# Kernel optimization log

Hardware: AMD Instinct MI355X
Metric: run time of the kernel (lower is better)

The kernel has to match this reference:

```python
import jax, jax.numpy as jnp
import numpy as np

COEF_MEMORY = 0.2

def setup_inputs() -> dict:
    key = jax.random.key(0)
    k1, k2, k3, k4 = jax.random.split(key, 4)
    B, T, HW, C, Cv, M = 2, 8, 4096, 64, 3, 1024
    k = jax.random.normal(k1, (B, T, HW, C), dtype=jnp.float32)
    v = jax.random.normal(k2, (B, T, HW, Cv), dtype=jnp.float32)
    m_k = jax.random.normal(k3, (B, T - 1, M, C), dtype=jnp.float32)
    m_v = jax.random.normal(k4, (B, T - 1, M, Cv), dtype=jnp.float32)
    return {"k": k, "v": v, "m_k": m_k, "m_v": m_v}

def reference(k, v, m_k, m_v):
    # k: [B,T,HW,C] frame keys; v: [B,T,HW,Cv] frame values (quarter-res images)
    # m_k: [B,T-1,M,C] memory keys at step i; m_v: [B,T-1,M,Cv] memory values
    c = COEF_MEMORY
    k_i = k[:, :-1]  # ref keys  [B,T-1,HW,C]
    k_j = k[:, 1:]   # tar keys  [B,T-1,HW,C]
    v_i = v[:, :-1]  # ref vals  [B,T-1,HW,Cv]
    # frame-to-frame affinity: softmax over ref positions (last axis)
    sim_k = jax.nn.softmax(jnp.einsum('btqc,btkc->btqk', k_j, k_i), axis=-1)
    # memory-to-frame affinity: softmax over memory slots
    sim_m = jax.nn.softmax(jnp.einsum('btqc,btmc->btqm', k_j, m_k), axis=-1)
    rec_k = jnp.einsum('btqk,btkd->btqd', sim_k, v_i)   # [B,T-1,HW,Cv]
    rec_m = jnp.einsum('btqm,btmd->btqd', sim_m, m_v)   # [B,T-1,HW,Cv]
    return (1.0 - c) * rec_k + c * rec_m
```

## Files before the change

### kernel.cpp

```cpp
#include <hip/hip_runtime.h>

typedef __attribute__((ext_vector_type(2))) __fp16 h2;
typedef __attribute__((ext_vector_type(4))) __fp16 h4;
typedef __attribute__((ext_vector_type(8))) __fp16 h8;
typedef __attribute__((ext_vector_type(4))) float f32x4;

#define LOG2E 1.44269504088896340736f

#define WS_K    0ull
#define WS_MK   7340032ull
#define WS_VT   9175040ull
#define WS_MVT  9633792ull
#define WS_NEED 9748480ull

__device__ __forceinline__ h2 pkrtz(float a, float b) {
    return __builtin_bit_cast(h2, __builtin_amdgcn_cvt_pkrtz(a, b));
}

__device__ __forceinline__ void gll16(const void* g, void* l) {
    __builtin_amdgcn_global_load_lds(
        (const __attribute__((address_space(1))) unsigned int*)g,
        (__attribute__((address_space(3))) unsigned int*)l, 16, 0, 0);
}

__global__ __launch_bounds__(256) void kast_pre_kernel(
    const float* __restrict__ K, const float* __restrict__ V,
    const float* __restrict__ MK, const float* __restrict__ MV,
    char* __restrict__ ws)
{
    const int id = blockIdx.x * 256 + threadIdx.x;
    if (id < 573440) {
        const bool ismk = id >= 458752;
        const int lid = ismk ? id - 458752 : id;
        const int c = lid & 7;
        const int r = (lid >> 3) & 63;
        int kt, s;
        if (ismk) { kt = (lid >> 9) & 15; s = lid >> 13; }
        else      { kt = (lid >> 9) & 63; s = lid >> 15; }
        const int b = s / 7, t = s - b * 7;
        const float* src = ismk
            ? MK + (((size_t)(b * 7 + t) * 1024 + kt * 64 + r) * 64 + c * 8)
            : K  + (((size_t)(b * 8 + t) * 4096 + kt * 64 + r) * 64 + c * 8);
        const f32x4 xa = *(const f32x4*)src;
        const f32x4 xb = *(const f32x4*)(src + 4);
        const h2 q0 = pkrtz(xa[0], xa[1]), q1 = pkrtz(xa[2], xa[3]);
        const h2 q2 = pkrtz(xb[0], xb[1]), q3 = pkrtz(xb[2], xb[3]);
        const h8 out = {q0[0], q0[1], q1[0], q1[1], q2[0], q2[1], q3[0], q3[1]};
        __fp16* dst = (__fp16*)(ws + (ismk ? WS_MK : WS_K))
                    + (size_t)(ismk ? (s * 16 + kt) : (s * 64 + kt)) * 4096
                    + r * 64 + ((c ^ (r & 7)) * 8);
        *(h8*)dst = out;
    } else {
        const int vid = id - 573440;
        const bool ismv = vid >= 57344;
        const int lid = ismv ? vid - 57344 : vid;
        const int c = lid & 15;
        const int d = (lid >> 4) & 3;
        int kt, s;
        if (ismv) { kt = (lid >> 6) & 15; s = lid >> 10; }
        else      { kt = (lid >> 6) & 63; s = lid >> 12; }
        const int b = s / 7, t = s - b * 7;
        const float* src = ismv
            ? MV + (((size_t)(b * 7 + t) * 1024 + kt * 64 + c * 4) * 3)
            : V  + (((size_t)(b * 8 + t) * 4096 + kt * 64 + c * 4) * 3);
        float f0, f1, f2, f3;
        if (d == 3) { f0 = f1 = f2 = f3 = 1.0f; }
        else { f0 = src[d]; f1 = src[3 + d]; f2 = src[6 + d]; f3 = src[9 + d]; }
        const h2 pa = pkrtz(f0, f1), pb = pkrtz(f2, f3);
        const h4 out4 = {pa[0], pa[1], pb[0], pb[1]};
        __fp16* dst = (__fp16*)(ws + (ismv ? WS_MVT : WS_VT))
                    + (size_t)(ismv ? (s * 16 + kt) : (s * 64 + kt)) * 256
                    + d * 64 + (4 * ((c >> 2) ^ d) + (c & 3)) * 4;
        *(h4*)dst = out4;
    }
}

__global__ __launch_bounds__(512) void kast_attn_kernel(
    const float* __restrict__ K,
    const char* __restrict__ ws,
    float* __restrict__ OUT)
{
    __shared__ alignas(16) __fp16 sK2[2][2][64][64];
    __shared__ alignas(16) __fp16 sVT2[2][2][4][64];
    __shared__ float mrg[8][32][5];

    const int id = blockIdx.x;
    const int sw = (id & 7) * 112 + (id >> 3);
    const int bt = sw >> 6;
    const int qblk = sw & 63;
    const int b = bt / 7, t = bt - b * 7;

    const int tid = threadIdx.x;
    const int lane = tid & 63;
    const int w = tid >> 6;
    const int h = w >> 2;
    const int wl = w & 3;
    const int qsub = wl >> 1;
    const int ntp = wl & 1;
    const int col = lane & 15;
    const int g = lane >> 4;
    const int cs = col & 7;
    const int d3 = col & 3;

    h8 aq[2][2];
#pragma unroll
    for (int mt = 0; mt < 2; ++mt) {
        const float* qp = K + (((size_t)b * 8 + (t + 1)) * 4096
                         + (size_t)(qblk * 64 + qsub * 32 + mt * 16 + col)) * 64;
#pragma unroll
        for (int ch = 0; ch < 2; ++ch) {
            const int cc = ch * 32 + g * 8;
            const f32x4 xa = *(const f32x4*)&qp[cc];
            const f32x4 xb = *(const f32x4*)&qp[cc + 4];
            const h2 p0 = pkrtz(xa[0] * LOG2E, xa[1] * LOG2E);
            const h2 p1 = pkrtz(xa[2] * LOG2E, xa[3] * LOG2E);
            const h2 p2 = pkrtz(xb[0] * LOG2E, xb[1] * LOG2E);
            const h2 p3 = pkrtz(xb[2] * LOG2E, xb[3] * LOG2E);
            aq[mt][ch] = (h8){p0[0], p0[1], p1[0], p1[1], p2[0], p2[1], p3[0], p3[1]};
        }
    }

    auto stage = [&](const char* kb, const char* vb, int tkt, int buf) {
        const char* ksrc = kb + (size_t)tkt * 8192 + wl * 2048 + lane * 16;
        char* kdst = ((char*)&sK2[h][buf][0][0]) + wl * 2048 + lane * 16;
        gll16(ksrc, kdst);
        gll16(ksrc + 1024, kdst + 1024);
        if (wl == 0 && lane < 32)
            ((f32x4*)&sVT2[h][buf][0][0])[lane] =
                ((const f32x4*)(vb + (size_t)tkt * 512))[lane];
    };

    float oa0 = 0.f, oa1 = 0.f, oa2 = 0.f;

#pragma unroll
    for (int phase = 0; phase < 2; ++phase) {
        const char* kbase; const char* vbase; int ntile; float wgt;
        if (phase == 0) {
            ntile = 32; wgt = 0.8f;
            kbase = ws + WS_K  + ((size_t)bt * 64 + h * 32) * 8192;
            vbase = ws + WS_VT + ((size_t)bt * 64 + h * 32) * 512;
        } else {
            ntile = 8; wgt = 0.2f;
            kbase = ws + WS_MK  + ((size_t)bt * 16 + h * 8) * 8192;
            vbase = ws + WS_MVT + ((size_t)bt * 16 + h * 8) * 512;
        }

        stage(kbase, vbase, 0, 0);
        __syncthreads();

        float mrun[2] = {-1e30f, -1e30f};
        f32x4 O[2] = {(f32x4){0.f,0.f,0.f,0.f}, (f32x4){0.f,0.f,0.f,0.f}};

        for (int kt = 0; kt < ntile; ++kt) {
            const int cur = kt & 1;

            if (kt + 1 < ntile) stage(kbase, vbase, kt + 1, cur ^ 1);

            f32x4 acc[2][2];
#pragma unroll
            for (int mt = 0; mt < 2; ++mt)
#pragma unroll
                for (int nt = 0; nt < 2; ++nt) acc[mt][nt] = (f32x4){0.f,0.f,0.f,0.f};
            __builtin_amdgcn_s_setprio(1);
#pragma unroll
            for (int ch = 0; ch < 2; ++ch) {
                h8 bh[2];
#pragma unroll
                for (int nt = 0; nt < 2; ++nt) {
                    const int nt2 = ntp * 2 + nt;
                    bh[nt] = *(const h8*)&sK2[h][cur][nt2 * 16 + col][((ch * 4 + g) ^ cs) * 8];
                }
#pragma unroll
                for (int mt = 0; mt < 2; ++mt)
#pragma unroll
                    for (int nt = 0; nt < 2; ++nt)
                        acc[mt][nt] = __builtin_amdgcn_mfma_f32_16x16x32_f16(bh[nt], aq[mt][ch], acc[mt][nt], 0, 0, 0);
            }
            __builtin_amdgcn_s_setprio(0);

            const char* vtb = (const char*)&sVT2[h][cur][0][0] + d3 * 128;
#pragma unroll
            for (int mt = 0; mt < 2; ++mt) {
                float tm = acc[mt][0][0];
#pragma unroll
                for (int nt = 0; nt < 2; ++nt)
#pragma unroll
                    for (int j = 0; j < 4; ++j) tm = fmaxf(tm, acc[mt][nt][j]);
                tm = fmaxf(tm, __shfl_xor(tm, 16));
                tm = fmaxf(tm, __shfl_xor(tm, 32));
                if (!__all(tm <= mrun[mt])) {
                    const float mnew = fmaxf(mrun[mt], tm);
                    const float sc = __builtin_amdgcn_exp2f(mrun[mt] - mnew);
                    O[mt] *= sc;
                    mrun[mt] = mnew;
                }
#pragma unroll
                for (int nt = 0; nt < 2; ++nt) {
                    const int nt2 = ntp * 2 + nt;
                    const float p0 = __builtin_amdgcn_exp2f(acc[mt][nt][0] - mrun[mt]);
                    const float p1 = __builtin_amdgcn_exp2f(acc[mt][nt][1] - mrun[mt]);
                    const float p2 = __builtin_amdgcn_exp2f(acc[mt][nt][2] - mrun[mt]);
                    const float p3 = __builtin_amdgcn_exp2f(acc[mt][nt][3] - mrun[mt]);
                    const h2 pa = pkrtz(p0, p1), pb = pkrtz(p2, p3);
                    const h4 pf = (h4){pa[0], pa[1], pb[0], pb[1]};
                    const h4 vf = *(const h4*)(vtb + (4 * (nt2 ^ d3) + g) * 8);
                    O[mt] = __builtin_amdgcn_mfma_f32_16x16x16f16(vf, pf, O[mt], 0, 0, 0);
                }
            }

            __syncthreads();
        }

        if (g == 0) {
#pragma unroll
            for (int mt = 0; mt < 2; ++mt) {
                float* m5 = &mrg[w][mt * 16 + col][0];
                m5[0] = mrun[mt];
                m5[1] = O[mt][0]; m5[2] = O[mt][1]; m5[3] = O[mt][2]; m5[4] = O[mt][3];
            }
        }
        __syncthreads();
        if (tid < 64) {
            const int qh = tid >> 5, ql = tid & 31;
            float m = -1e30f;
#pragma unroll
            for (int c = 0; c < 4; ++c) {
                const int w4 = (c >> 1) * 4 + qh * 2 + (c & 1);
                m = fmaxf(m, mrg[w4][ql][0]);
            }
            float l = 0.f, r0 = 0.f, r1 = 0.f, r2 = 0.f;
#pragma unroll
            for (int c = 0; c < 4; ++c) {
                const int w4 = (c >> 1) * 4 + qh * 2 + (c & 1);
                const float* m5 = &mrg[w4][ql][0];
                const float e = __builtin_amdgcn_exp2f(m5[0] - m);
                r0 += m5[1] * e; r1 += m5[2] * e; r2 += m5[3] * e;
                l  += m5[4] * e;
            }
            const float inv = wgt / l;
            oa0 += r0 * inv; oa1 += r1 * inv; oa2 += r2 * inv;
        }
    }

    if (tid < 64) {
        const int q = qblk * 64 + tid;
        float* op = OUT + (((size_t)b * 7 + t) * 4096 + (size_t)q) * 3;
        op[0] = oa0; op[1] = oa1; op[2] = oa2;
    }
}

__global__ __launch_bounds__(256) void kast_attn_fb(
    const float* __restrict__ K, const float* __restrict__ V,
    const float* __restrict__ MK, const float* __restrict__ MV,
    float* __restrict__ OUT)
{
    __shared__ alignas(16) __fp16 sK[2][64][64];
    __shared__ alignas(16) __fp16 sVT[2][4][68];

    const int id = blockIdx.x;
    const int sw = (id & 7) * 112 + (id >> 3);
    const int bt = sw >> 6;
    const int qblk = sw & 63;
    const int b = bt / 7, t = bt % 7;

    const int tid = threadIdx.x;
    const int lane = tid & 63;
    const int w = tid >> 6;
    const int col = lane & 15;
    const int g = lane >> 4;

    const int r = tid >> 2;
    const int c0 = (tid & 3) * 16;
    const int rs = (r & 7) << 3;
    const unsigned vr = (unsigned)tid / 3u;
    const unsigned vd = (unsigned)tid - vr * 3u;

    if (tid < 128) sVT[tid >> 6][3][tid & 63] = (__fp16)1.0f;

    const float* Qbase = K + (((size_t)b * 8 + (t + 1)) * 4096) * 64;
    h8 aq[2];
    {
        const int qrow = qblk * 64 + w * 16 + col;
        const float* qp = Qbase + (size_t)qrow * 64;
#pragma unroll
        for (int ch = 0; ch < 2; ++ch) {
            const int cc = ch * 32 + g * 8;
            const f32x4 xa = *(const f32x4*)&qp[cc];
            const f32x4 xb = *(const f32x4*)&qp[cc + 4];
            const h2 p0 = pkrtz(xa[0] * LOG2E, xa[1] * LOG2E);
            const h2 p1 = pkrtz(xa[2] * LOG2E, xa[3] * LOG2E);
            const h2 p2 = pkrtz(xb[0] * LOG2E, xb[1] * LOG2E);
            const h2 p3 = pkrtz(xb[2] * LOG2E, xb[3] * LOG2E);
            aq[ch] = (h8){p0[0], p0[1], p1[0], p1[1], p2[0], p2[1], p3[0], p3[1]};
        }
    }

    float outc0 = 0.f, outc1 = 0.f, outc2 = 0.f;

    for (int phase = 0; phase < 2; ++phase) {
        const float* kp; const float* vp; int ntile; float wgt;
        if (phase == 0) {
            kp = K + (((size_t)b * 8 + t) * 4096) * 64;
            vp = V + (((size_t)b * 8 + t) * 4096) * 3;
            ntile = 64; wgt = 0.8f;
        } else {
            kp = MK + (((size_t)b * 7 + t) * 1024) * 64;
            vp = MV + (((size_t)b * 7 + t) * 1024) * 3;
            ntile = 16; wgt = 0.2f;
        }
        {
            const float* src = kp + ((size_t)r) * 64 + c0;
            const f32x4* s4 = (const f32x4*)src;
            const f32x4 ra = s4[0], rb = s4[1], rc = s4[2], rd = s4[3];
            const h2 q0 = pkrtz(ra[0], ra[1]), q1 = pkrtz(ra[2], ra[3]);
            const h2 q2 = pkrtz(rb[0], rb[1]), q3 = pkrtz(rb[2], rb[3]);
            const h2 q4 = pkrtz(rc[0], rc[1]), q5 = pkrtz(rc[2], rc[3]);
            const h2 q6 = pkrtz(rd[0], rd[1]), q7 = pkrtz(rd[2], rd[3]);
            *(h8*)&sK[0][r][c0 ^ rs] = (h8){q0[0], q0[1], q1[0], q1[1], q2[0], q2[1], q3[0], q3[1]};
            *(h8*)&sK[0][r][(c0 + 8) ^ rs] = (h8){q4[0], q4[1], q5[0], q5[1], q6[0], q6[1], q7[0], q7[1]};
            if (tid < 192) sVT[0][vd][vr] = (__fp16)vp[tid];
        }
        __syncthreads();

        float mrun = -1e30f;
        f32x4 O = (f32x4){0.f, 0.f, 0.f, 0.f};

        for (int kt = 0; kt < ntile; ++kt) {
            const int cur = kt & 1;
            const bool have = (kt + 1) < ntile;
            f32x4 ra, rb, rc, rd; float rv = 0.f;
            if (have) {
                const float* src = kp + ((size_t)(kt + 1) * 64 + r) * 64 + c0;
                const f32x4* s4 = (const f32x4*)src;
                ra = s4[0]; rb = s4[1]; rc = s4[2]; rd = s4[3];
                if (tid < 192) rv = vp[(size_t)(kt + 1) * 192 + tid];
            }
            f32x4 acc[4];
#pragma unroll
            for (int nt = 0; nt < 4; ++nt) acc[nt] = (f32x4){0.f, 0.f, 0.f, 0.f};
#pragma unroll
            for (int ch = 0; ch < 2; ++ch) {
                h8 bh[4];
#pragma unroll
                for (int nt = 0; nt < 4; ++nt) {
                    const int rr = nt * 16 + col;
                    const int cc = (ch * 32 + g * 8) ^ ((rr & 7) << 3);
                    bh[nt] = *(const h8*)&sK[cur][rr][cc];
                }
#pragma unroll
                for (int nt = 0; nt < 4; ++nt)
                    acc[nt] = __builtin_amdgcn_mfma_f32_16x16x32_f16(bh[nt], aq[ch], acc[nt], 0, 0, 0);
            }
            {
                float tm = acc[0][0];
#pragma unroll
                for (int nt = 0; nt < 4; ++nt)
#pragma unroll
                    for (int j = 0; j < 4; ++j) tm = fmaxf(tm, acc[nt][j]);
                tm = fmaxf(tm, __shfl_xor(tm, 16));
                tm = fmaxf(tm, __shfl_xor(tm, 32));
                if (!__all(tm <= mrun)) {
                    const float mnew = fmaxf(mrun, tm);
                    const float sc = __builtin_amdgcn_exp2f(mrun - mnew);
                    O *= sc;
                    mrun = mnew;
                }
            }
#pragma unroll
            for (int nt = 0; nt < 4; ++nt) {
                const float p0 = __builtin_amdgcn_exp2f(acc[nt][0] - mrun);
                const float p1 = __builtin_amdgcn_exp2f(acc[nt][1] - mrun);
                const float p2 = __builtin_amdgcn_exp2f(acc[nt][2] - mrun);
                const float p3 = __builtin_amdgcn_exp2f(acc[nt][3] - mrun);
                const h2 pa = pkrtz(p0, p1), pb = pkrtz(p2, p3);
                const h4 pf = (h4){pa[0], pa[1], pb[0], pb[1]};
                const h4 vf = *(const h4*)&sVT[cur][col & 3][nt * 16 + 4 * g];
                O = __builtin_amdgcn_mfma_f32_16x16x16f16(vf, pf, O, 0, 0, 0);
            }
            if (have) {
                const int nb = cur ^ 1;
                const h2 q0 = pkrtz(ra[0], ra[1]), q1 = pkrtz(ra[2], ra[3]);
                const h2 q2 = pkrtz(rb[0], rb[1]), q3 = pkrtz(rb[2], rb[3]);
                const h2 q4 = pkrtz(rc[0], rc[1]), q5 = pkrtz(rc[2], rc[3]);
                const h2 q6 = pkrtz(rd[0], rd[1]), q7 = pkrtz(rd[2], rd[3]);
                *(h8*)&sK[nb][r][c0 ^ rs] = (h8){q0[0], q0[1], q1[0], q1[1], q2[0], q2[1], q3[0], q3[1]};
                *(h8*)&sK[nb][r][(c0 + 8) ^ rs] = (h8){q4[0], q4[1], q5[0], q5[1], q6[0], q6[1], q7[0], q7[1]};
                if (tid < 192) sVT[nb][vd][vr] = (__fp16)rv;
            }
            __syncthreads();
        }
        const float inv = wgt / O[3];
        outc0 += O[0] * inv;
        outc1 += O[1] * inv;
        outc2 += O[2] * inv;
    }

    if (g == 0) {
        const int q = qblk * 64 + w * 16 + col;
        float* op = OUT + (((size_t)b * 7 + t) * 4096 + (size_t)q) * 3;
        op[0] = outc0; op[1] = outc1; op[2] = outc2;
    }
}

extern "C" void kernel_launch(void* const* d_in, const int* in_sizes, int n_in,
                              void* d_out, int out_size, void* d_ws, size_t ws_size,
                              hipStream_t stream) {
    const float* K  = (const float*)d_in[0];
    const float* V  = (const float*)d_in[1];
    const float* MK = (const float*)d_in[2];
    const float* MV = (const float*)d_in[3];
    float* OUT = (float*)d_out;
    if (ws_size >= WS_NEED) {
        hipLaunchKernelGGL(kast_pre_kernel, dim3(2520), dim3(256), 0, stream,
                           K, V, MK, MV, (char*)d_ws);
        hipLaunchKernelGGL(kast_attn_kernel, dim3(896), dim3(512), 0, stream,
                           K, (const char*)d_ws, OUT);
    } else {
        hipLaunchKernelGGL(kast_attn_fb, dim3(896), dim3(256), 0, stream,
                           K, V, MK, MV, OUT);
    }
}
```

Baseline: 118.1 us.

## Split keys across waves with private LDS buffers and drop per-tile block barriers

Restructures the attention kernel from 512 threads (two key halves × four waves sharing tiles) to 256 threads where each wave owns a contiguous key segment and all 64 queries, staging its own K tiles into a private LDS double buffer. This removes the per-tile __syncthreads and replaces it with explicit vmcnt waits. V fragments are now loaded straight from global memory into registers and prefetched one tile ahead. The lazy max-rescale branch is also replaced with an unconditional rescale. The intent is to cut barrier stalls and raise MFMA reuse of each K fragment, at the cost of more registers per wave, fewer waves per block, and hand-written wait counts that must match the outstanding loads.

```diff
diff --git a/kernel.cpp b/kernel.cpp
--- a/kernel.cpp
+++ b/kernel.cpp
@@ -75,14 +75,13 @@
     }
 }
 
-__global__ __launch_bounds__(512) void kast_attn_kernel(
+__global__ __launch_bounds__(256) void kast_attn_kernel(
     const float* __restrict__ K,
     const char* __restrict__ ws,
     float* __restrict__ OUT)
 {
-    __shared__ alignas(16) __fp16 sK2[2][2][64][64];
-    __shared__ alignas(16) __fp16 sVT2[2][2][4][64];
-    __shared__ float mrg[8][32][5];
+    __shared__ alignas(16) __fp16 sKp[4][2][32][64];
+    __shared__ float mrg[4][64][5];
 
     const int id = blockIdx.x;
     const int sw = (id & 7) * 112 + (id >> 3);
@@ -93,20 +92,16 @@
     const int tid = threadIdx.x;
     const int lane = tid & 63;
     const int w = tid >> 6;
-    const int h = w >> 2;
-    const int wl = w & 3;
-    const int qsub = wl >> 1;
-    const int ntp = wl & 1;
     const int col = lane & 15;
     const int g = lane >> 4;
     const int cs = col & 7;
     const int d3 = col & 3;
 
-    h8 aq[2][2];
-#pragma unroll
-    for (int mt = 0; mt < 2; ++mt) {
+    h8 aq[4][2];
+#pragma unroll
+    for (int mt = 0; mt < 4; ++mt) {
         const float* qp = K + (((size_t)b * 8 + (t + 1)) * 4096
-                         + (size_t)(qblk * 64 + qsub * 32 + mt * 16 + col)) * 64;
+                         + (size_t)(qblk * 64 + mt * 16 + col)) * 64;
 #pragma unroll
         for (int ch = 0; ch < 2; ++ch) {
             const int cc = ch * 32 + g * 8;
@@ -120,45 +115,57 @@
         }
     }
 
-    auto stage = [&](const char* kb, const char* vb, int tkt, int buf) {
-        const char* ksrc = kb + (size_t)tkt * 8192 + wl * 2048 + lane * 16;
-        char* kdst = ((char*)&sK2[h][buf][0][0]) + wl * 2048 + lane * 16;
-        gll16(ksrc, kdst);
-        gll16(ksrc + 1024, kdst + 1024);
-        if (wl == 0 && lane < 32)
-            ((f32x4*)&sVT2[h][buf][0][0])[lane] =
-                ((const f32x4*)(vb + (size_t)tkt * 512))[lane];
-    };
-
     float oa0 = 0.f, oa1 = 0.f, oa2 = 0.f;
 
 #pragma unroll
     for (int phase = 0; phase < 2; ++phase) {
-        const char* kbase; const char* vbase; int ntile; float wgt;
-        if (phase == 0) {
-            ntile = 32; wgt = 0.8f;
-            kbase = ws + WS_K  + ((size_t)bt * 64 + h * 32) * 8192;
-            vbase = ws + WS_VT + ((size_t)bt * 64 + h * 32) * 512;
-        } else {
-            ntile = 8; wgt = 0.2f;
-            kbase = ws + WS_MK  + ((size_t)bt * 16 + h * 8) * 8192;
-            vbase = ws + WS_MVT + ((size_t)bt * 16 + h * 8) * 512;
-        }
-
-        stage(kbase, vbase, 0, 0);
-        __syncthreads();
-
-        float mrun[2] = {-1e30f, -1e30f};
-        f32x4 O[2] = {(f32x4){0.f,0.f,0.f,0.f}, (f32x4){0.f,0.f,0.f,0.f}};
-
-        for (int kt = 0; kt < ntile; ++kt) {
+        const int n = phase ? 8 : 32;
+        const float wgt = phase ? 0.2f : 0.8f;
+        const int keys_off = w * (phase ? 256 : 1024);
+        const char* kseg = ws + (phase ? (WS_MK + (size_t)bt * 16 * 8192)
+                                       : (WS_K  + (size_t)bt * 64 * 8192))
+                         + (size_t)keys_off * 128;
+        const char* vseg = ws + (phase ? (WS_MVT + (size_t)bt * 16 * 512)
+                                       : (WS_VT  + (size_t)bt * 64 * 512))
+                         + (size_t)(keys_off >> 6) * 512;
+
+        {
+            const char* ksrc = kseg + lane * 16;
+            char* kdst = ((char*)&sKp[w][0][0][0]) + lane * 16;
+#pragma unroll
+            for (int i = 0; i < 4; ++i) gll16(ksrc + i * 1024, kdst + i * 1024);
+        }
+        const char* vt0 = vseg + d3 * 128;
+        h4 v0 = *(const h4*)(vt0 + (4 * (0 ^ d3) + g) * 8);
+        h4 v1 = *(const h4*)(vt0 + (4 * (1 ^ d3) + g) * 8);
+
+        float mrun[4] = {-1e30f, -1e30f, -1e30f, -1e30f};
+        f32x4 O[4];
+#pragma unroll
+        for (int mt = 0; mt < 4; ++mt) O[mt] = (f32x4){0.f, 0.f, 0.f, 0.f};
+
+        for (int kt = 0; kt < n; ++kt) {
             const int cur = kt & 1;
-
-            if (kt + 1 < ntile) stage(kbase, vbase, kt + 1, cur ^ 1);
-
-            f32x4 acc[2][2];
-#pragma unroll
-            for (int mt = 0; mt < 2; ++mt)
+            h4 nv0 = v0, nv1 = v1;
+
+            if (kt + 1 < n) {
+                const char* ksrc = kseg + (size_t)(kt + 1) * 4096 + lane * 16;
+                char* kdst = ((char*)&sKp[w][cur ^ 1][0][0]) + lane * 16;
+#pragma unroll
+                for (int i = 0; i < 4; ++i) gll16(ksrc + i * 1024, kdst + i * 1024);
+                const int sub = (kt + 1) & 1;
+                const char* vt = vseg + (size_t)((kt + 1) >> 1) * 512 + d3 * 128;
+                nv0 = *(const h4*)(vt + (4 * ((sub * 2 + 0) ^ d3) + g) * 8);
+                nv1 = *(const h4*)(vt + (4 * ((sub * 2 + 1) ^ d3) + g) * 8);
+                asm volatile("s_waitcnt vmcnt(6)" ::: "memory");
+            } else {
+                asm volatile("s_waitcnt vmcnt(0)" ::: "memory");
+            }
+            __builtin_amdgcn_sched_barrier(0);
+
+            f32x4 acc[4][2];
+#pragma unroll
+            for (int mt = 0; mt < 4; ++mt)
 #pragma unroll
                 for (int nt = 0; nt < 2; ++nt) acc[mt][nt] = (f32x4){0.f,0.f,0.f,0.f};
             __builtin_amdgcn_s_setprio(1);
@@ -166,54 +173,51 @@
             for (int ch = 0; ch < 2; ++ch) {
                 h8 bh[2];
 #pragma unroll
-                for (int nt = 0; nt < 2; ++nt) {
-                    const int nt2 = ntp * 2 + nt;
-                    bh[nt] = *(const h8*)&sK2[h][cur][nt2 * 16 + col][((ch * 4 + g) ^ cs) * 8];
-                }
-#pragma unroll
-                for (int mt = 0; mt < 2; ++mt)
+                for (int nt = 0; nt < 2; ++nt)
+                    bh[nt] = *(const h8*)&sKp[w][cur][nt * 16 + col][((ch * 4 + g) ^ cs) * 8];
+#pragma unroll
+                for (int mt = 0; mt < 4; ++mt)
 #pragma unroll
                     for (int nt = 0; nt < 2; ++nt)
                         acc[mt][nt] = __builtin_amdgcn_mfma_f32_16x16x32_f16(bh[nt], aq[mt][ch], acc[mt][nt], 0, 0, 0);
             }
             __builtin_amdgcn_s_setprio(0);
 
-            const char* vtb = (const char*)&sVT2[h][cur][0][0] + d3 * 128;
-#pragma unroll
-            for (int mt = 0; mt < 2; ++mt) {
-                float tm = acc[mt][0][0];
-#pragma unroll
-                for (int nt = 0; nt < 2; ++nt)
-#pragma unroll
-                    for (int j = 0; j < 4; ++j) tm = fmaxf(tm, acc[mt][nt][j]);
+#pragma unroll
+            for (int mt = 0; mt < 4; ++mt) {
+                float tm = fmaxf(fmaxf(fmaxf(acc[mt][0][0], acc[mt][0][1]),
+                                       fmaxf(acc[mt][0][2], acc[mt][0][3])),
+                                 fmaxf(fmaxf(acc[mt][1][0], acc[mt][1][1]),
+                                       fmaxf(acc[mt][1][2], acc[mt][1][3])));
                 tm = fmaxf(tm, __shfl_xor(tm, 16));
                 tm = fmaxf(tm, __shfl_xor(tm, 32));
-                if (!__all(tm <= mrun[mt])) {
-                    const float mnew = fmaxf(mrun[mt], tm);
-                    const float sc = __builtin_amdgcn_exp2f(mrun[mt] - mnew);
-                    O[mt] *= sc;
-                    mrun[mt] = mnew;
-                }
-#pragma unroll
-                for (int nt = 0; nt < 2; ++nt) {
-                    const int nt2 = ntp * 2 + nt;
+                const float m = fmaxf(mrun[mt], tm);
+                const float sc = __builtin_amdgcn_exp2f(mrun[mt] - m);
+                O[mt] *= sc;
+                mrun[mt] = m;
+            }
+
+#pragma unroll
+            for (int nt = 0; nt < 2; ++nt) {
+                const h4 vf = nt ? v1 : v0;
+#pragma unroll
+                for (int mt = 0; mt < 4; ++mt) {
                     const float p0 = __builtin_amdgcn_exp2f(acc[mt][nt][0] - mrun[mt]);
                     const float p1 = __builtin_amdgcn_exp2f(acc[mt][nt][1] - mrun[mt]);
                     const float p2 = __builtin_amdgcn_exp2f(acc[mt][nt][2] - mrun[mt]);
                     const float p3 = __builtin_amdgcn_exp2f(acc[mt][nt][3] - mrun[mt]);
                     const h2 pa = pkrtz(p0, p1), pb = pkrtz(p2, p3);
                     const h4 pf = (h4){pa[0], pa[1], pb[0], pb[1]};
-                    const h4 vf = *(const h4*)(vtb + (4 * (nt2 ^ d3) + g) * 8);
                     O[mt] = __builtin_amdgcn_mfma_f32_16x16x16f16(vf, pf, O[mt], 0, 0, 0);
                 }
             }
 
-            __syncthreads();
+            v0 = nv0; v1 = nv1;
         }
 
         if (g == 0) {
 #pragma unroll
-            for (int mt = 0; mt < 2; ++mt) {
+            for (int mt = 0; mt < 4; ++mt) {
                 float* m5 = &mrg[w][mt * 16 + col][0];
                 m5[0] = mrun[mt];
                 m5[1] = O[mt][0]; m5[2] = O[mt][1]; m5[3] = O[mt][2]; m5[4] = O[mt][3];
@@ -221,18 +225,13 @@
         }
         __syncthreads();
         if (tid < 64) {
-            const int qh = tid >> 5, ql = tid & 31;
             float m = -1e30f;
 #pragma unroll
-            for (int c = 0; c < 4; ++c) {
-                const int w4 = (c >> 1) * 4 + qh * 2 + (c & 1);
-                m = fmaxf(m, mrg[w4][ql][0]);
-            }
+            for (int q4 = 0; q4 < 4; ++q4) m = fmaxf(m, mrg[q4][tid][0]);
             float l = 0.f, r0 = 0.f, r1 = 0.f, r2 = 0.f;
 #pragma unroll
-            for (int c = 0; c < 4; ++c) {
-                const int w4 = (c >> 1) * 4 + qh * 2 + (c & 1);
-                const float* m5 = &mrg[w4][ql][0];
+            for (int q4 = 0; q4 < 4; ++q4) {
+                const float* m5 = &mrg[q4][tid][0];
                 const float e = __builtin_amdgcn_exp2f(m5[0] - m);
                 r0 += m5[1] * e; r1 += m5[2] * e; r2 += m5[3] * e;
                 l  += m5[4] * e;
@@ -240,6 +239,7 @@
             const float inv = wgt / l;
             oa0 += r0 * inv; oa1 += r1 * inv; oa2 += r2 * inv;
         }
+        __syncthreads();
     }
 
     if (tid < 64) {
@@ -413,7 +413,7 @@
     if (ws_size >= WS_NEED) {
         hipLaunchKernelGGL(kast_pre_kernel, dim3(2520), dim3(256), 0, stream,
                            K, V, MK, MV, (char*)d_ws);
-        hipLaunchKernelGGL(kast_attn_kernel, dim3(896), dim3(512), 0, stream,
+        hipLaunchKernelGGL(kast_attn_kernel, dim3(896), dim3(256), 0, stream,
                            K, (const char*)d_ws, OUT);
     } else {
         hipLaunchKernelGGL(kast_attn_fb, dim3(896), dim3(256), 0, stream,
```

Result: no change. 119.6 us (+1.3%).
